# Performance work log

Measured on AMD Instinct MI355X. Metric: run time of the kernel, lower is better.

Reference implementation:

```python
import jax, jax.numpy as jnp
import numpy as np

N_NODES = 10000
N_EDGES = 640000
D = 128
BN_EPS = 1e-5


def setup_inputs() -> dict:
    key = jax.random.key(0)
    k1, k2, k3 = jax.random.split(key, 3)
    x = jax.random.normal(k1, (N_NODES, D), dtype=jnp.float32)
    edge_index = jax.random.randint(k2, (2, N_EDGES), 0, N_NODES, dtype=jnp.int64)
    W = jax.random.normal(k3, (D, D), dtype=jnp.float32) * (1.0 / np.sqrt(D))
    b = jnp.zeros((D,), dtype=jnp.float32)
    gamma = jnp.ones((D,), dtype=jnp.float32)
    beta = jnp.zeros((D,), dtype=jnp.float32)
    return {"x": x, "edge_index": edge_index, "W": W, "b": b, "gamma": gamma, "beta": beta}


def reference(x, edge_index, W, b, gamma, beta):
    # GINConv: out_i = MLP((1+eps)*x_i + sum_{j->i} x_j), eps=0
    src = edge_index[0]
    dst = edge_index[1]
    agg = jax.ops.segment_sum(x[src], dst, num_segments=N_NODES)  # [N, D]
    h = agg + x  # (1 + eps) * x with eps = 0
    # MLP inside GINConv: Linear + ReLU
    h = jnp.maximum(h @ W + b, 0.0)
    # outer F.relu (idempotent after inner ReLU, kept for faithfulness)
    h = jnp.maximum(h, 0.0)
    # BatchNorm1d, training-mode batch statistics (biased variance)
    mean = jnp.mean(h, axis=0)
    var = jnp.var(h, axis=0)
    h = (h - mean) * jax.lax.rsqrt(var + BN_EPS) * gamma + beta
    # Dropout in eval mode -> identity. his_x = [h]; return the main output.
    return h
```

## Files before the change

### kernel.cpp

```cpp
#include <hip/hip_runtime.h>

#define N_NODES 10000
#define N_EDGES 640000
#define D 128
#define BN_EPS 1e-5f
#define CAP 128
#define NSTRIPE 16
#define RPB 8
#define NB 1250
#define BCAP 704
#define ABLK 128
#define ASLICE 5000
#define CSENT 1250

typedef _Float16 half8_t __attribute__((ext_vector_type(8)));
typedef unsigned short u16;

__global__ __launch_bounds__(256) void k_bin(
    const int* __restrict__ ei,
    const float4* __restrict__ x4,
    int* cur,
    int* __restrict__ recs,
    half8_t* __restrict__ xh)
{
    __shared__ int cnt[NB];
    __shared__ int base[NB];
    const int b = blockIdx.x, t = threadIdx.x;

    {
        const int n8 = N_NODES * D / 8;
        for (int i = b * 256 + t; i < n8; i += ABLK * 256) {
            const float4 a = x4[2 * i];
            const float4 c = x4[2 * i + 1];
            half8_t h;
            h[0] = (_Float16)a.x; h[1] = (_Float16)a.y;
            h[2] = (_Float16)a.z; h[3] = (_Float16)a.w;
            h[4] = (_Float16)c.x; h[5] = (_Float16)c.y;
            h[6] = (_Float16)c.z; h[7] = (_Float16)c.w;
            xh[i] = h;
        }
    }

    for (int i = t; i < NB; i += 256) cnt[i] = 0;
    __syncthreads();

    const int e0 = b * ASLICE;
    for (int i = t; i < ASLICE; i += 256)
        atomicAdd(&cnt[ei[N_EDGES + e0 + i] >> 3], 1);
    __syncthreads();

    const unsigned cbase = (unsigned)cur[CSENT];
    for (int i = t; i < NB; i += 256) {
        const int c = cnt[i];
        base[i] = (int)((unsigned)atomicAdd(&cur[i], c) - cbase);
        cnt[i] = 0;
    }
    __syncthreads();

    for (int i = t; i < ASLICE; i += 256) {
        const int e = e0 + i;
        const int d = ei[N_EDGES + e];
        const int s = ei[e];
        const int bin = d >> 3;
        const int p = base[bin] + atomicAdd(&cnt[bin], 1);
        if (p < BCAP) recs[bin * BCAP + p] = (s << 3) | (d & 7);
    }
}

__global__ __launch_bounds__(256) void k_gfill(
    const float* __restrict__ x,
    const half8_t* __restrict__ xh8,
    const int* __restrict__ cur,
    const int* __restrict__ recs,
    const float* __restrict__ W,
    const float* __restrict__ bias,
    float* __restrict__ out,
    float* __restrict__ stats)
{
    __shared__ u16 lst[RPB * CAP];
    __shared__ int cnt[RPB];
    __shared__ float hs[RPB][D];
    const int tid  = threadIdx.x;
    const int bin  = blockIdx.x;
    const int wv   = tid >> 6;
    const int lane = tid & 63;
    const int qq   = lane >> 4;
    const int l    = lane & 15;
    const float4* __restrict__ x4 = (const float4*)x;

    if (tid < RPB) cnt[tid] = 0;
    __syncthreads();

    const unsigned cbase = (unsigned)cur[CSENT];
    int nrec = (int)((unsigned)cur[bin] - cbase);
    if (nrec > BCAP) nrec = BCAP;
    const int* __restrict__ br = recs + bin * BCAP;
    for (int i = tid; i < nrec; i += 256) {
        const int r = br[i];
        const int p = atomicAdd(&cnt[r & 7], 1);
        if (p < CAP) lst[(r & 7) * CAP + p] = (u16)(r >> 3);
    }
    __syncthreads();

    #pragma unroll
    for (int j = 0; j < 2; j++) {
        const int lrow = wv * 2 + j;
        const int node = bin * RPB + lrow;
        int n = cnt[lrow];
        if (n > CAP) n = CAP;
        const u16* __restrict__ myl = &lst[lrow * CAP];
        float acc[8];
        #pragma unroll
        for (int z = 0; z < 8; z++) acc[z] = 0.f;

        int i = 0;
        for (; i + 64 <= n; i += 64) {
            const int sj = (int)myl[i + lane];
            #pragma unroll
            for (int b = 0; b < 2; b++) {
                half8_t v[8];
                #pragma unroll
                for (int u = 0; u < 8; u++) {
                    const int s = __shfl(sj, 4 * (b * 8 + u) + qq, 64);
                    v[u] = xh8[(size_t)s * 16 + l];
                }
                #pragma unroll
                for (int u = 0; u < 8; u++)
                    #pragma unroll
                    for (int z = 0; z < 8; z++)
                        acc[z] += (float)v[u][z];
            }
        }
        const int c = n - i;
        if (c > 0) {
            const int sj = (lane < c) ? (int)myl[i + lane] : 0;
            const int quads = c >> 2;
            for (int t2 = 0; t2 < quads; t2 += 8) {
                half8_t v[8];
                #pragma unroll
                for (int u = 0; u < 8; u++) {
                    const int s = __shfl(sj, (4 * (t2 + u) + qq) & 63, 64);
                    v[u] = xh8[(size_t)s * 16 + l];
                }
                #pragma unroll
                for (int u = 0; u < 8; u++) {
                    if (t2 + u < quads) {
                        #pragma unroll
                        for (int z = 0; z < 8; z++)
                            acc[z] += (float)v[u][z];
                    }
                }
            }
            const int r = c & 3;
            if (r > 0) {
                const int s = __shfl(sj, (4 * quads + qq) & 63, 64);
                const half8_t vv = xh8[(size_t)s * 16 + l];
                if (qq < r) {
                    #pragma unroll
                    for (int z = 0; z < 8; z++)
                        acc[z] += (float)vv[z];
                }
            }
        }
        #pragma unroll
        for (int z = 0; z < 8; z++) {
            acc[z] += __shfl_xor(acc[z], 16, 64);
            acc[z] += __shfl_xor(acc[z], 32, 64);
        }
        if (qq == 0) {
            const float4 xa = x4[(size_t)node * 32 + 2 * l];
            const float4 xb = x4[(size_t)node * 32 + 2 * l + 1];
            *(float4*)&hs[lrow][8 * l] =
                make_float4(acc[0] + xa.x, acc[1] + xa.y, acc[2] + xa.z, acc[3] + xa.w);
            *(float4*)&hs[lrow][8 * l + 4] =
                make_float4(acc[4] + xb.x, acc[5] + xb.y, acc[6] + xb.z, acc[7] + xb.w);
        }
    }
    __syncthreads();

    const int col = tid & 127;
    const int rg  = tid >> 7;
    float a[4] = {0.f, 0.f, 0.f, 0.f};
    #pragma unroll 8
    for (int k = 0; k < D; k++) {
        const float w = W[k * D + col];
        #pragma unroll
        for (int r = 0; r < 4; r++)
            a[r] = fmaf(hs[rg * 4 + r][k], w, a[r]);
    }

    const float bcol = bias[col];
    float s1 = 0.f, s2 = 0.f;
    #pragma unroll
    for (int r = 0; r < 4; r++) {
        const float v = fmaxf(a[r] + bcol, 0.f);
        out[(size_t)(bin * RPB + rg * 4 + r) * D + col] = v;
        s1 += v;
        s2 += v * v;
    }

    __syncthreads();
    float* red = &hs[0][0];
    red[tid]       = s1;
    red[256 + tid] = s2;
    __syncthreads();
    if (tid < D) {
        float* sp = &stats[(size_t)(bin & (NSTRIPE - 1)) * 256];
        atomicAdd(&sp[tid],     red[tid]       + red[tid + 128]);
        atomicAdd(&sp[D + tid], red[256 + tid] + red[256 + tid + 128]);
    }
}

__global__ __launch_bounds__(256) void k_bn(
    float* out,
    const float* __restrict__ stats,
    const float* __restrict__ gamma,
    const float* __restrict__ beta)
{
    __shared__ float sc[D], sh[D];
    const int tid = threadIdx.x;
    if (tid < D) {
        const float fbase = stats[NSTRIPE * 256];
        float s = 0.f, q = 0.f;
        #pragma unroll
        for (int cp = 0; cp < NSTRIPE; cp++) {
            s += stats[cp * 256 + tid]     - fbase;
            q += stats[cp * 256 + D + tid] - fbase;
        }
        const float mean = s * (1.0f / N_NODES);
        const float var  = q * (1.0f / N_NODES) - mean * mean;
        const float scale = gamma[tid] * rsqrtf(var + BN_EPS);
        sc[tid] = scale;
        sh[tid] = beta[tid] - mean * scale;
    }
    __syncthreads();

    float4* o4 = (float4*)out;
    #pragma unroll
    for (int j = 0; j < 2; j++) {
        const int f = blockIdx.x * 512 + j * 256 + tid;
        const int c = (f & 31) << 2;
        float4 v = o4[f];
        v.x = v.x * sc[c]     + sh[c];
        v.y = v.y * sc[c + 1] + sh[c + 1];
        v.z = v.z * sc[c + 2] + sh[c + 2];
        v.w = v.w * sc[c + 3] + sh[c + 3];
        o4[f] = v;
    }
}

extern "C" void kernel_launch(void* const* d_in, const int* in_sizes, int n_in,
                              void* d_out, int out_size, void* d_ws, size_t ws_size,
                              hipStream_t stream)
{
    const float* x     = (const float*)d_in[0];
    const int*   ei    = (const int*)d_in[1];
    const float* W     = (const float*)d_in[2];
    const float* bias  = (const float*)d_in[3];
    const float* gamma = (const float*)d_in[4];
    const float* beta  = (const float*)d_in[5];
    float* out = (float*)d_out;

    float*   stats = (float*)d_ws;
    int*     cur   = (int*)(stats + NSTRIPE * 256 + 8);
    int*     recs  = cur + 1280;
    half8_t* xh    = (half8_t*)(recs + NB * BCAP);

    k_bin<<<ABLK, 256, 0, stream>>>(ei, (const float4*)x, cur, recs, xh);
    k_gfill<<<NB, 256, 0, stream>>>(x, xh, cur, recs, W, bias, out, stats);
    k_bn<<<N_NODES * D / 2048, 256, 0, stream>>>(out, stats, gamma, beta);
}
```

Measured before the change: 118.6 us.

## Fuse BatchNorm into gather kernel with last-block grid sync and per-block binning

```diff
diff --git a/kernel.cpp b/kernel.cpp
--- a/kernel.cpp
+++ b/kernel.cpp
@@ -6,247 +6,280 @@
 #define BN_EPS 1e-5f
 #define CAP 128
 #define NSTRIPE 16
-#define RPB 8
 #define NB 1250
-#define BCAP 704
+#define SLOT 16
 #define ABLK 128
-#define ASLICE 5000
-#define CSENT 1250
+#define ESLICE 5000
+#define OVFCAP 1024
+#define GFB 625
 
 typedef _Float16 half8_t __attribute__((ext_vector_type(8)));
 typedef unsigned short u16;
+
+__device__ __forceinline__ int ldA(const int* p) {
+    return __hip_atomic_load(p, __ATOMIC_RELAXED, __HIP_MEMORY_SCOPE_AGENT);
+}
+__device__ __forceinline__ float ldAf(const float* p) {
+    return __hip_atomic_load(p, __ATOMIC_RELAXED, __HIP_MEMORY_SCOPE_AGENT);
+}
+__device__ __forceinline__ void stAf(float* p, float v) {
+    __hip_atomic_store(p, v, __ATOMIC_RELEASE, __HIP_MEMORY_SCOPE_AGENT);
+}
 
 __global__ __launch_bounds__(256) void k_bin(
     const int* __restrict__ ei,
     const float4* __restrict__ x4,
-    int* cur,
+    int* ctrl,
+    int* __restrict__ cntg,
     int* __restrict__ recs,
+    int* __restrict__ ovf,
     half8_t* __restrict__ xh)
 {
     __shared__ int cnt[NB];
-    __shared__ int base[NB];
     const int b = blockIdx.x, t = threadIdx.x;
 
-    {
-        const int n8 = N_NODES * D / 8;
-        for (int i = b * 256 + t; i < n8; i += ABLK * 256) {
-            const float4 a = x4[2 * i];
-            const float4 c = x4[2 * i + 1];
-            half8_t h;
-            h[0] = (_Float16)a.x; h[1] = (_Float16)a.y;
-            h[2] = (_Float16)a.z; h[3] = (_Float16)a.w;
-            h[4] = (_Float16)c.x; h[5] = (_Float16)c.y;
-            h[6] = (_Float16)c.z; h[7] = (_Float16)c.w;
-            xh[i] = h;
-        }
+    const int n8 = N_NODES * D / 8;
+    for (int i = b * 256 + t; i < n8; i += ABLK * 256) {
+        const float4 a = x4[2 * i], c = x4[2 * i + 1];
+        half8_t h;
+        h[0] = (_Float16)a.x; h[1] = (_Float16)a.y;
+        h[2] = (_Float16)a.z; h[3] = (_Float16)a.w;
+        h[4] = (_Float16)c.x; h[5] = (_Float16)c.y;
+        h[6] = (_Float16)c.z; h[7] = (_Float16)c.w;
+        xh[i] = h;
     }
 
     for (int i = t; i < NB; i += 256) cnt[i] = 0;
     __syncthreads();
 
-    const int e0 = b * ASLICE;
-    for (int i = t; i < ASLICE; i += 256)
-        atomicAdd(&cnt[ei[N_EDGES + e0 + i] >> 3], 1);
-    __syncthreads();
-
-    const unsigned cbase = (unsigned)cur[CSENT];
-    for (int i = t; i < NB; i += 256) {
-        const int c = cnt[i];
-        base[i] = (int)((unsigned)atomicAdd(&cur[i], c) - cbase);
-        cnt[i] = 0;
-    }
-    __syncthreads();
-
-    for (int i = t; i < ASLICE; i += 256) {
+    const unsigned base = (unsigned)ldA(&ctrl[2]);
+    const int e0 = b * ESLICE;
+    for (int i = t; i < ESLICE; i += 256) {
         const int e = e0 + i;
         const int d = ei[N_EDGES + e];
         const int s = ei[e];
         const int bin = d >> 3;
-        const int p = base[bin] + atomicAdd(&cnt[bin], 1);
-        if (p < BCAP) recs[bin * BCAP + p] = (s << 3) | (d & 7);
-    }
-}
-
-__global__ __launch_bounds__(256) void k_gfill(
+        const int p = atomicAdd(&cnt[bin], 1);
+        if (p < SLOT) {
+            recs[(bin << 11) + (b << 4) + p] = (s << 3) | (d & 7);
+        } else {
+            const unsigned o = (unsigned)atomicAdd(&ctrl[3], 1) - base;
+            if (o < OVFCAP) ovf[o] = (d << 14) | s;
+        }
+    }
+    __syncthreads();
+    for (int i = t; i < NB; i += 256) cntg[b * NB + i] = min(cnt[i], SLOT);
+}
+
+__global__ __launch_bounds__(256, 4) void k_gfill(
     const float* __restrict__ x,
     const half8_t* __restrict__ xh8,
-    const int* __restrict__ cur,
+    const int* __restrict__ cntg,
     const int* __restrict__ recs,
+    const int* __restrict__ ovf,
+    int* ctrl,
     const float* __restrict__ W,
     const float* __restrict__ bias,
+    const float* __restrict__ gamma,
+    const float* __restrict__ beta,
     float* __restrict__ out,
-    float* __restrict__ stats)
+    float* stats,
+    float* bnp)
 {
-    __shared__ u16 lst[RPB * CAP];
-    __shared__ int cnt[RPB];
-    __shared__ float hs[RPB][D];
+    __shared__ u16 lst[8 * CAP];
+    __shared__ int cnt[8];
+    __shared__ float hs[8][D];
+    __shared__ int amLast;
     const int tid  = threadIdx.x;
-    const int bin  = blockIdx.x;
-    const int wv   = tid >> 6;
-    const int lane = tid & 63;
-    const int qq   = lane >> 4;
-    const int l    = lane & 15;
+    const int wv   = tid >> 6, lane = tid & 63;
+    const int qq   = lane >> 4, l = lane & 15;
+    const int col  = tid & 127, rg = tid >> 7;
     const float4* __restrict__ x4 = (const float4*)x;
-
-    if (tid < RPB) cnt[tid] = 0;
-    __syncthreads();
-
-    const unsigned cbase = (unsigned)cur[CSENT];
-    int nrec = (int)((unsigned)cur[bin] - cbase);
-    if (nrec > BCAP) nrec = BCAP;
-    const int* __restrict__ br = recs + bin * BCAP;
-    for (int i = tid; i < nrec; i += 256) {
-        const int r = br[i];
-        const int p = atomicAdd(&cnt[r & 7], 1);
-        if (p < CAP) lst[(r & 7) * CAP + p] = (u16)(r >> 3);
-    }
-    __syncthreads();
-
-    #pragma unroll
-    for (int j = 0; j < 2; j++) {
-        const int lrow = wv * 2 + j;
-        const int node = bin * RPB + lrow;
-        int n = cnt[lrow];
-        if (n > CAP) n = CAP;
-        const u16* __restrict__ myl = &lst[lrow * CAP];
-        float acc[8];
-        #pragma unroll
-        for (int z = 0; z < 8; z++) acc[z] = 0.f;
-
-        int i = 0;
-        for (; i + 64 <= n; i += 64) {
-            const int sj = (int)myl[i + lane];
+    const unsigned base = (unsigned)ldA(&ctrl[2]);
+
+    float hreg[8];
+    float s1 = 0.f, s2 = 0.f;
+
+    for (int ib = 0; ib < 2; ib++) {
+        const int bin = blockIdx.x * 2 + ib;
+        if (tid < 8) cnt[tid] = 0;
+        __syncthreads();
+
+        {
+            const int blk = tid >> 1, hf = tid & 1;
+            const int c = cntg[blk * NB + bin];
+            const int* rr = recs + (bin << 11) + (blk << 4);
+            const int k1 = (c < hf * 8 + 8) ? c : hf * 8 + 8;
+            for (int k = hf * 8; k < k1; k++) {
+                const int r = rr[k];
+                const int p = atomicAdd(&cnt[r & 7], 1);
+                if (p < CAP) lst[(r & 7) * CAP + p] = (u16)(r >> 3);
+            }
+        }
+        {
+            int novf = (int)((unsigned)ldA(&ctrl[3]) - base);
+            if (novf > 0) {
+                if (novf > OVFCAP) novf = OVFCAP;
+                for (int i = tid; i < novf; i += 256) {
+                    const int v = ovf[i];
+                    const int node = v >> 14;
+                    if ((node >> 3) == bin) {
+                        const int p = atomicAdd(&cnt[node & 7], 1);
+                        if (p < CAP) lst[(node & 7) * CAP + p] = (u16)(v & 0x3FFF);
+                    }
+                }
+            }
+        }
+        __syncthreads();
+
+        for (int j = 0; j < 2; j++) {
+            const int lrow = wv * 2 + j;
+            const int node = bin * 8 + lrow;
+            int n = cnt[lrow]; if (n > CAP) n = CAP;
+            const u16* __restrict__ myl = &lst[lrow * CAP];
+            float acc[8];
             #pragma unroll
-            for (int b = 0; b < 2; b++) {
-                half8_t v[8];
+            for (int z = 0; z < 8; z++) acc[z] = 0.f;
+
+            int i = 0;
+            for (; i + 64 <= n; i += 64) {
+                const int sj = (int)myl[i + lane];
                 #pragma unroll
-                for (int u = 0; u < 8; u++) {
-                    const int s = __shfl(sj, 4 * (b * 8 + u) + qq, 64);
-                    v[u] = xh8[(size_t)s * 16 + l];
-                }
-                #pragma unroll
-                for (int u = 0; u < 8; u++)
+                for (int b2 = 0; b2 < 2; b2++) {
+                    half8_t v[8];
                     #pragma unroll
-                    for (int z = 0; z < 8; z++)
-                        acc[z] += (float)v[u][z];
-            }
-        }
-        const int c = n - i;
-        if (c > 0) {
-            const int sj = (lane < c) ? (int)myl[i + lane] : 0;
-            const int quads = c >> 2;
-            for (int t2 = 0; t2 < quads; t2 += 8) {
-                half8_t v[8];
-                #pragma unroll
-                for (int u = 0; u < 8; u++) {
-                    const int s = __shfl(sj, (4 * (t2 + u) + qq) & 63, 64);
-                    v[u] = xh8[(size_t)s * 16 + l];
-                }
-                #pragma unroll
-                for (int u = 0; u < 8; u++) {
-                    if (t2 + u < quads) {
+                    for (int u = 0; u < 8; u++) {
+                        const int s = __shfl(sj, 4 * (b2 * 8 + u) + qq, 64);
+                        v[u] = xh8[(size_t)s * 16 + l];
+                    }
+                    #pragma unroll
+                    for (int u = 0; u < 8; u++)
                         #pragma unroll
                         for (int z = 0; z < 8; z++)
                             acc[z] += (float)v[u][z];
-                    }
                 }
             }
-            const int r = c & 3;
-            if (r > 0) {
-                const int s = __shfl(sj, (4 * quads + qq) & 63, 64);
-                const half8_t vv = xh8[(size_t)s * 16 + l];
-                if (qq < r) {
+            const int c = n - i;
+            if (c > 0) {
+                const int sj = (lane < c) ? (int)myl[i + lane] : 0;
+                const int quads = c >> 2;
+                for (int t2 = 0; t2 < quads; t2 += 8) {
+                    half8_t v[8];
                     #pragma unroll
-                    for (int z = 0; z < 8; z++)
-                        acc[z] += (float)vv[z];
+                    for (int u = 0; u < 8; u++) {
+                        const int s = __shfl(sj, (4 * (t2 + u) + qq) & 63, 64);
+                        v[u] = xh8[(size_t)s * 16 + l];
+                    }
+                    #pragma unroll
+                    for (int u = 0; u < 8; u++) {
+                        if (t2 + u < quads) {
+                            #pragma unroll
+                            for (int z = 0; z < 8; z++)
+                                acc[z] += (float)v[u][z];
+                        }
+                    }
                 }
-            }
-        }
+                const int r = c & 3;
+                if (r > 0) {
+                    const int s = __shfl(sj, (4 * quads + qq) & 63, 64);
+                    const half8_t vv = xh8[(size_t)s * 16 + l];
+                    if (qq < r) {
+                        #pragma unroll
+                        for (int z = 0; z < 8; z++)
+                            acc[z] += (float)vv[z];
+                    }
+                }
+            }
+            #pragma unroll
+            for (int z = 0; z < 8; z++) {
+                acc[z] += __shfl_xor(acc[z], 16, 64);
+                acc[z] += __shfl_xor(acc[z], 32, 64);
+            }
+            if (qq == 0) {
+                const float4 xa = x4[(size_t)node * 32 + 2 * l];
+                const float4 xb = x4[(size_t)node * 32 + 2 * l + 1];
+                *(float4*)&hs[lrow][8 * l] =
+                    make_float4(acc[0] + xa.x, acc[1] + xa.y, acc[2] + xa.z, acc[3] + xa.w);
+                *(float4*)&hs[lrow][8 * l + 4] =
+                    make_float4(acc[4] + xb.x, acc[5] + xb.y, acc[6] + xb.z, acc[7] + xb.w);
+            }
+        }
+        __syncthreads();
+
+        float a[4] = {0.f, 0.f, 0.f, 0.f};
+        #pragma unroll 8
+        for (int k = 0; k < D; k++) {
+            const float w = W[k * D + col];
+            #pragma unroll
+            for (int r = 0; r < 4; r++)
+                a[r] = fmaf(hs[rg * 4 + r][k], w, a[r]);
+        }
+        const float bcol = bias[col];
         #pragma unroll
-        for (int z = 0; z < 8; z++) {
-            acc[z] += __shfl_xor(acc[z], 16, 64);
-            acc[z] += __shfl_xor(acc[z], 32, 64);
-        }
-        if (qq == 0) {
-            const float4 xa = x4[(size_t)node * 32 + 2 * l];
-            const float4 xb = x4[(size_t)node * 32 + 2 * l + 1];
-            *(float4*)&hs[lrow][8 * l] =
-                make_float4(acc[0] + xa.x, acc[1] + xa.y, acc[2] + xa.z, acc[3] + xa.w);
-            *(float4*)&hs[lrow][8 * l + 4] =
-                make_float4(acc[4] + xb.x, acc[5] + xb.y, acc[6] + xb.z, acc[7] + xb.w);
-        }
-    }
-    __syncthreads();
-
-    const int col = tid & 127;
-    const int rg  = tid >> 7;
-    float a[4] = {0.f, 0.f, 0.f, 0.f};
-    #pragma unroll 8
-    for (int k = 0; k < D; k++) {
-        const float w = W[k * D + col];
-        #pragma unroll
-        for (int r = 0; r < 4; r++)
-            a[r] = fmaf(hs[rg * 4 + r][k], w, a[r]);
-    }
-
-    const float bcol = bias[col];
-    float s1 = 0.f, s2 = 0.f;
-    #pragma unroll
-    for (int r = 0; r < 4; r++) {
-        const float v = fmaxf(a[r] + bcol, 0.f);
-        out[(size_t)(bin * RPB + rg * 4 + r) * D + col] = v;
-        s1 += v;
-        s2 += v * v;
-    }
-
-    __syncthreads();
+        for (int r = 0; r < 4; r++) {
+            const float v = fmaxf(a[r] + bcol, 0.f);
+            hreg[ib * 4 + r] = v;
+            s1 += v;
+            s2 += v * v;
+        }
+        __syncthreads();
+    }
+
     float* red = &hs[0][0];
     red[tid]       = s1;
     red[256 + tid] = s2;
     __syncthreads();
     if (tid < D) {
-        float* sp = &stats[(size_t)(bin & (NSTRIPE - 1)) * 256];
+        float* sp = &stats[(size_t)(blockIdx.x & (NSTRIPE - 1)) * 256];
         atomicAdd(&sp[tid],     red[tid]       + red[tid + 128]);
         atomicAdd(&sp[D + tid], red[256 + tid] + red[256 + tid + 128]);
     }
-}
-
-__global__ __launch_bounds__(256) void k_bn(
-    float* out,
-    const float* __restrict__ stats,
-    const float* __restrict__ gamma,
-    const float* __restrict__ beta)
-{
-    __shared__ float sc[D], sh[D];
-    const int tid = threadIdx.x;
-    if (tid < D) {
-        const float fbase = stats[NSTRIPE * 256];
-        float s = 0.f, q = 0.f;
+    __threadfence();
+    __syncthreads();
+    if (tid == 0) {
+        const unsigned old = (unsigned)__hip_atomic_fetch_add(
+            &ctrl[0], 1, __ATOMIC_ACQ_REL, __HIP_MEMORY_SCOPE_AGENT);
+        amLast = (old - base == GFB - 1);
+    }
+    __syncthreads();
+
+    if (amLast) {
+        if (tid < D) {
+            float s = 0.f, q = 0.f;
+            #pragma unroll
+            for (int cp = 0; cp < NSTRIPE; cp++) {
+                s += ldAf(&stats[cp * 256 + tid]);
+                q += ldAf(&stats[cp * 256 + D + tid]);
+            }
+            const float mean = s * (1.0f / N_NODES);
+            const float var  = q * (1.0f / N_NODES) - mean * mean;
+            const float sc = gamma[tid] * rsqrtf(var + BN_EPS);
+            stAf(&bnp[tid], sc);
+            stAf(&bnp[D + tid], beta[tid] - mean * sc);
+        }
+        __threadfence();
+        __syncthreads();
+        if (tid == 0)
+            __hip_atomic_store(&ctrl[1], (int)(base + 1), __ATOMIC_RELEASE,
+                               __HIP_MEMORY_SCOPE_AGENT);
+    } else {
+        if (tid == 0) {
+            while ((unsigned)ldA(&ctrl[1]) == base)
+                __builtin_amdgcn_s_sleep(32);
+            (void)__hip_atomic_load(&ctrl[1], __ATOMIC_ACQUIRE,
+                                    __HIP_MEMORY_SCOPE_AGENT);
+        }
+        __syncthreads();
+    }
+
+    const float sc = ldAf(&bnp[col]);
+    const float sh = ldAf(&bnp[D + col]);
+    #pragma unroll
+    for (int ib = 0; ib < 2; ib++)
         #pragma unroll
-        for (int cp = 0; cp < NSTRIPE; cp++) {
-            s += stats[cp * 256 + tid]     - fbase;
-            q += stats[cp * 256 + D + tid] - fbase;
-        }
-        const float mean = s * (1.0f / N_NODES);
-        const float var  = q * (1.0f / N_NODES) - mean * mean;
-        const float scale = gamma[tid] * rsqrtf(var + BN_EPS);
-        sc[tid] = scale;
-        sh[tid] = beta[tid] - mean * scale;
-    }
-    __syncthreads();
-
-    float4* o4 = (float4*)out;
-    #pragma unroll
-    for (int j = 0; j < 2; j++) {
-        const int f = blockIdx.x * 512 + j * 256 + tid;
-        const int c = (f & 31) << 2;
-        float4 v = o4[f];
-        v.x = v.x * sc[c]     + sh[c];
-        v.y = v.y * sc[c + 1] + sh[c + 1];
-        v.z = v.z * sc[c + 2] + sh[c + 2];
-        v.w = v.w * sc[c + 3] + sh[c + 3];
-        o4[f] = v;
-    }
+        for (int r = 0; r < 4; r++)
+            out[(size_t)(blockIdx.x * 16 + ib * 8 + rg * 4 + r) * D + col] =
+                hreg[ib * 4 + r] * sc + sh;
 }
 
 extern "C" void kernel_launch(void* const* d_in, const int* in_sizes, int n_in,
@@ -261,12 +294,16 @@
     const float* beta  = (const float*)d_in[5];
     float* out = (float*)d_out;
 
-    float*   stats = (float*)d_ws;
-    int*     cur   = (int*)(stats + NSTRIPE * 256 + 8);
-    int*     recs  = cur + 1280;
-    half8_t* xh    = (half8_t*)(recs + NB * BCAP);
-
-    k_bin<<<ABLK, 256, 0, stream>>>(ei, (const float4*)x, cur, recs, xh);
-    k_gfill<<<NB, 256, 0, stream>>>(x, xh, cur, recs, W, bias, out, stats);
-    k_bn<<<N_NODES * D / 2048, 256, 0, stream>>>(out, stats, gamma, beta);
-}
+    char* p = (char*)d_ws;
+    int*     ctrl  = (int*)p;                 p += 32;
+    float*   bnp   = (float*)p;               p += 256 * 4;
+    float*   stats = (float*)p;               p += NSTRIPE * 256 * 4;
+    int*     cntg  = (int*)p;                 p += (size_t)ABLK * NB * 4;
+    int*     ovf   = (int*)p;                 p += OVFCAP * 4;
+    int*     recs  = (int*)p;                 p += (size_t)NB * ABLK * SLOT * 4;
+    half8_t* xh    = (half8_t*)p;
+
+    k_bin<<<ABLK, 256, 0, stream>>>(ei, (const float4*)x, ctrl, cntg, recs, ovf, xh);
+    k_gfill<<<GFB, 256, 0, stream>>>(x, xh, cntg, recs, ovf, ctrl,
+                                     W, bias, gamma, beta, out, stats, bnp);
+}
```

Measured after the change: 241.6 us. 104% more time.
